# Optimization experiments

Measured on AMD Instinct MI355X. Metric: run time of the kernel, lower is better.

Reference implementation:

```python
import jax, jax.numpy as jnp
import numpy as np

B, S, DIM, SECL = 32, 2048, 1024, 16  # dim = 2*hidden_dim


def setup_inputs() -> dict:
    key = jax.random.key(0)
    ks = jax.random.split(key, 10)
    return {
        "dec_hidden": jax.random.normal(ks[0], (B, DIM), jnp.float32),
        "enc_output": jax.random.normal(ks[1], (B, S, DIM), jnp.float32),
        "enc_feature": jax.random.normal(ks[2], (B, S, DIM), jnp.float32),
        "enc_mask": jnp.ones((B, S), jnp.float32),
        "sec_attn": jax.random.uniform(ks[3], (B, SECL), jnp.float32),
        "coverage": jax.random.uniform(ks[4], (B, S), jnp.float32),
        "W_dec": jax.random.normal(ks[5], (DIM, DIM), jnp.float32) * (1.0 / np.sqrt(DIM)),
        "b_dec": jax.random.normal(ks[6], (DIM,), jnp.float32) * 0.01,
        "v": jax.random.normal(ks[7], (DIM,), jnp.float32) * (1.0 / np.sqrt(DIM)),
        "w_cov": jax.random.normal(ks[8], (DIM,), jnp.float32) * 0.1,
    }


def reference(dec_hidden, enc_output, enc_feature, enc_mask, sec_attn, coverage,
              W_dec, b_dec, v, w_cov):
    # dec_feature: [B, dim], broadcast over src_len
    dec_feature = dec_hidden @ W_dec.T + b_dec
    # att_features = enc_feature + dec_feature + coverage * w_cov  -> [B, S, dim]
    att = enc_feature + dec_feature[:, None, :] + coverage[:, :, None] * w_cov[None, None, :]
    # scalar score per position: v . tanh(att)  -> [B, S]
    score = jnp.einsum('bsd,d->bs', jnp.tanh(att), v)
    # NOTE: the original multiplies sec_attn*score into attn_dist but immediately
    # overwrites it with softmax(score)*mask, so sec_attn does not affect outputs.
    attn = jax.nn.softmax(score, axis=1) * enc_mask
    attn = attn / jnp.sum(attn, axis=1, keepdims=True)
    # context = attn @ enc_output  -> [B, dim]
    context = jnp.einsum('bs,bsd->bd', attn, enc_output)
    coverage_new = coverage + attn
    return context, attn, coverage_new
```

## Files before the change

kernel.cpp:

```cpp
#include <hip/hip_runtime.h>

#define BB 32
#define SS 2048
#define DD 1024

typedef float f32x4 __attribute__((ext_vector_type(4)));

#if defined(__has_builtin)
#  if __has_builtin(__builtin_amdgcn_exp2f)
#    define EXP2F(x) __builtin_amdgcn_exp2f(x)
#  endif
#  if __has_builtin(__builtin_amdgcn_rcpf)
#    define RCPF(x) __builtin_amdgcn_rcpf(x)
#  endif
#endif
#ifndef EXP2F
#  define EXP2F(x) exp2f(x)
#endif
#ifndef RCPF
#  define RCPF(x) (1.0f / (x))
#endif

#define LOG2E 1.44269504088896340736f

__device__ __forceinline__ float fast_tanh(float x) {
    x = fminf(fmaxf(x, -20.0f), 20.0f);
    float e = EXP2F(x * (2.0f * LOG2E));
    return (e - 1.0f) * RCPF(e + 1.0f);
}

__device__ __forceinline__ f32x4 ntload4(const float* p) {
    return __builtin_nontemporal_load((const f32x4*)p);
}

__global__ __launch_bounds__(256) void k_decfeat(
    const float* __restrict__ dh, const float* __restrict__ W,
    const float* __restrict__ bd, float* __restrict__ df,
    float* __restrict__ ctx) {
    if (blockIdx.x < BB) {
        f32x4 z = {0.f, 0.f, 0.f, 0.f};
        ((f32x4*)ctx)[blockIdx.x * 256 + threadIdx.x] = z;
    }
    int wave = threadIdx.x >> 6;
    int lane = threadIdx.x & 63;
    int o = blockIdx.x * 4 + wave;
    int b = o >> 10, i = o & 1023;
    const float4* wrow = (const float4*)(W + (size_t)i * DD);
    const float4* drow = (const float4*)(dh + (size_t)b * DD);
    float acc = 0.0f;
#pragma unroll
    for (int r = 0; r < 4; ++r) {
        float4 w4 = wrow[lane + 64 * r];
        float4 d4 = drow[lane + 64 * r];
        acc += w4.x * d4.x + w4.y * d4.y + w4.z * d4.z + w4.w * d4.w;
    }
#pragma unroll
    for (int off = 32; off; off >>= 1) acc += __shfl_down(acc, off, 64);
    if (lane == 0) df[o] = acc + bd[i];
}

__global__ __launch_bounds__(256) void k_fused(
    const float* __restrict__ ef, const float* __restrict__ df,
    const float* __restrict__ cov, const float* __restrict__ v,
    const float* __restrict__ wc, const float* __restrict__ mask,
    const float* __restrict__ eo, float* __restrict__ attn_un,
    float* __restrict__ sum_part, float* __restrict__ ctx) {
    int b = blockIdx.x >> 5, ch = blockIdx.x & 31;
    int s0 = ch * 64;
    int t = threadIdx.x;
    int lane = t & 63, wave = t >> 6;
    float4 v4 = ((const float4*)v)[t];
    float4 w4 = ((const float4*)wc)[t];
    float4 d4 = ((const float4*)(df + (size_t)b * DD))[t];
    __shared__ float als[64];
    __shared__ float red[4][8];
    for (int sub = 0; sub < 8; ++sub) {
        int ss0 = s0 + sub * 8;
        float part[8];
#pragma unroll
        for (int k = 0; k < 8; ++k) {
            int s = ss0 + k;
            float c = cov[b * SS + s];
            f32x4 e4 = ntload4(ef + ((size_t)b * SS + s) * DD + t * 4);
            float t0 = fast_tanh(e4.x + d4.x + c * w4.x);
            float t1 = fast_tanh(e4.y + d4.y + c * w4.y);
            float t2 = fast_tanh(e4.z + d4.z + c * w4.z);
            float t3 = fast_tanh(e4.w + d4.w + c * w4.w);
            part[k] = v4.x * t0 + v4.y * t1 + v4.z * t2 + v4.w * t3;
        }
#pragma unroll
        for (int k = 0; k < 8; ++k) {
            float p = part[k];
#pragma unroll
            for (int off = 32; off; off >>= 1) p += __shfl_down(p, off, 64);
            if (lane == 0) red[wave][k] = p;
        }
        __syncthreads();
        if (t < 8) {
            float sc = red[0][t] + red[1][t] + red[2][t] + red[3][t];
            float em = EXP2F(sc * LOG2E) * mask[b * SS + ss0 + t];
            attn_un[b * SS + ss0 + t] = em;
            als[sub * 8 + t] = em;
        }
        __syncthreads();
    }
    if (t < 64) {
        float s = als[t];
#pragma unroll
        for (int off = 32; off; off >>= 1) s += __shfl_down(s, off, 64);
        if (t == 0) sum_part[b * 32 + ch] = s;
    }
    const float* base = eo + ((size_t)b * SS + s0) * DD;
    f32x4 acc = {0.f, 0.f, 0.f, 0.f};
#pragma unroll 8
    for (int k = 0; k < 64; ++k) {
        f32x4 e4 = ntload4(base + (size_t)k * DD + t * 4);
        acc += als[k] * e4;
    }
    float* cp = ctx + (size_t)b * DD + t * 4;
    atomicAdd(cp + 0, acc.x);
    atomicAdd(cp + 1, acc.y);
    atomicAdd(cp + 2, acc.z);
    atomicAdd(cp + 3, acc.w);
}

__global__ __launch_bounds__(256) void k_finalize(
    const float* __restrict__ sum_part, const float* __restrict__ cov,
    float* __restrict__ attn, float* __restrict__ covnew,
    float* __restrict__ ctx) {
    int b = blockIdx.x >> 3, dt = blockIdx.x & 7;
    int t = threadIdx.x;
    __shared__ float invs;
    if (t < 32) {
        float s = sum_part[b * 32 + t];
#pragma unroll
        for (int off = 16; off; off >>= 1) s += __shfl_down(s, off, 32);
        if (t == 0) invs = RCPF(s);
    }
    __syncthreads();
    float inv = invs;
    int s = dt * 256 + t;
    float a = attn[b * SS + s] * inv;
    attn[b * SS + s] = a;
    covnew[b * SS + s] = cov[b * SS + s] + a;
    if (t < 128) {
        int d = dt * 128 + t;
        ctx[(size_t)b * DD + d] *= inv;
    }
}

extern "C" void kernel_launch(void* const* d_in, const int* in_sizes, int n_in,
                              void* d_out, int out_size, void* d_ws, size_t ws_size,
                              hipStream_t stream) {
    const float* dec_hidden  = (const float*)d_in[0];
    const float* enc_output  = (const float*)d_in[1];
    const float* enc_feature = (const float*)d_in[2];
    const float* enc_mask    = (const float*)d_in[3];
    const float* coverage    = (const float*)d_in[5];
    const float* W_dec       = (const float*)d_in[6];
    const float* b_dec       = (const float*)d_in[7];
    const float* v           = (const float*)d_in[8];
    const float* w_cov       = (const float*)d_in[9];

    float* ctx    = (float*)d_out;
    float* attn   = (float*)d_out + BB * DD;
    float* covnew = (float*)d_out + BB * DD + BB * SS;

    char* ws = (char*)d_ws;
    float* df       = (float*)(ws);
    float* sum_part = (float*)(ws + 131072);

    k_decfeat  <<<8192,  256, 0, stream>>>(dec_hidden, W_dec, b_dec, df, ctx);
    k_fused    <<<BB*32, 256, 0, stream>>>(enc_feature, df, coverage, v, w_cov,
                                           enc_mask, enc_output, attn, sum_part, ctx);
    k_finalize <<<BB*8,  256, 0, stream>>>(sum_part, coverage, attn, covnew, ctx);
}
```

Measured before the change: 97.66 us.

## Fold finalize kernel into fused kernel via last-block-per-batch atomic counter

Removes the separate finalize launch. Each batch row now has an atomic completion counter, reset in the dec-feature kernel. The last of the 32 chunk blocks for a batch row normalizes attn, writes the new coverage and scales the context, with thread fences to order the writes. This saves a kernel launch and its gap, but puts the finalize work for each batch on a single block at the tail of the fused kernel and adds fences and atomics to every block.

```diff
diff --git a/kernel.cpp b/kernel.cpp
--- a/kernel.cpp
+++ b/kernel.cpp
@@ -36,10 +36,11 @@
 __global__ __launch_bounds__(256) void k_decfeat(
     const float* __restrict__ dh, const float* __restrict__ W,
     const float* __restrict__ bd, float* __restrict__ df,
-    float* __restrict__ ctx) {
+    float* __restrict__ ctx, int* __restrict__ done) {
     if (blockIdx.x < BB) {
         f32x4 z = {0.f, 0.f, 0.f, 0.f};
         ((f32x4*)ctx)[blockIdx.x * 256 + threadIdx.x] = z;
+        if (threadIdx.x == 0) done[blockIdx.x] = 0;
     }
     int wave = threadIdx.x >> 6;
     int lane = threadIdx.x & 63;
@@ -63,8 +64,9 @@
     const float* __restrict__ ef, const float* __restrict__ df,
     const float* __restrict__ cov, const float* __restrict__ v,
     const float* __restrict__ wc, const float* __restrict__ mask,
-    const float* __restrict__ eo, float* __restrict__ attn_un,
-    float* __restrict__ sum_part, float* __restrict__ ctx) {
+    const float* __restrict__ eo, float* __restrict__ attn,
+    float* __restrict__ covnew, float* __restrict__ sum_part,
+    float* __restrict__ ctx, int* __restrict__ done) {
     int b = blockIdx.x >> 5, ch = blockIdx.x & 31;
     int s0 = ch * 64;
     int t = threadIdx.x;
@@ -99,7 +101,7 @@
         if (t < 8) {
             float sc = red[0][t] + red[1][t] + red[2][t] + red[3][t];
             float em = EXP2F(sc * LOG2E) * mask[b * SS + ss0 + t];
-            attn_un[b * SS + ss0 + t] = em;
+            attn[b * SS + ss0 + t] = em;
             als[sub * 8 + t] = em;
         }
         __syncthreads();
@@ -122,14 +124,12 @@
     atomicAdd(cp + 1, acc.y);
     atomicAdd(cp + 2, acc.z);
     atomicAdd(cp + 3, acc.w);
-}
-
-__global__ __launch_bounds__(256) void k_finalize(
-    const float* __restrict__ sum_part, const float* __restrict__ cov,
-    float* __restrict__ attn, float* __restrict__ covnew,
-    float* __restrict__ ctx) {
-    int b = blockIdx.x >> 3, dt = blockIdx.x & 7;
-    int t = threadIdx.x;
+    __threadfence();
+    __shared__ int lastFlag;
+    if (t == 0) lastFlag = (atomicAdd(done + b, 1) == 31);
+    __syncthreads();
+    if (!lastFlag) return;
+    __threadfence();
     __shared__ float invs;
     if (t < 32) {
         float s = sum_part[b * 32 + t];
@@ -139,14 +139,15 @@
     }
     __syncthreads();
     float inv = invs;
-    int s = dt * 256 + t;
-    float a = attn[b * SS + s] * inv;
-    attn[b * SS + s] = a;
-    covnew[b * SS + s] = cov[b * SS + s] + a;
-    if (t < 128) {
-        int d = dt * 128 + t;
-        ctx[(size_t)b * DD + d] *= inv;
+#pragma unroll
+    for (int k = 0; k < 8; ++k) {
+        int s = t + 256 * k;
+        float a = attn[b * SS + s] * inv;
+        attn[b * SS + s] = a;
+        covnew[b * SS + s] = cov[b * SS + s] + a;
     }
+    f32x4* cp4 = (f32x4*)(ctx + (size_t)b * DD);
+    cp4[t] = cp4[t] * inv;
 }
 
 extern "C" void kernel_launch(void* const* d_in, const int* in_sizes, int n_in,
@@ -169,9 +170,10 @@
     char* ws = (char*)d_ws;
     float* df       = (float*)(ws);
     float* sum_part = (float*)(ws + 131072);
+    int*   done     = (int*)(ws + 131072 + 4096);
 
-    k_decfeat  <<<8192,  256, 0, stream>>>(dec_hidden, W_dec, b_dec, df, ctx);
-    k_fused    <<<BB*32, 256, 0, stream>>>(enc_feature, df, coverage, v, w_cov,
-                                           enc_mask, enc_output, attn, sum_part, ctx);
-    k_finalize <<<BB*8,  256, 0, stream>>>(sum_part, coverage, attn, covnew, ctx);
+    k_decfeat <<<8192,  256, 0, stream>>>(dec_hidden, W_dec, b_dec, df, ctx, done);
+    k_fused   <<<BB*32, 256, 0, stream>>>(enc_feature, df, coverage, v, w_cov,
+                                          enc_mask, enc_output, attn, covnew,
+                                          sum_part, ctx, done);
 }
```

After: 303.7 us. 3.11x slower.
